# Optimization experiments

Measured on AMD Instinct MI355X. Metric: run time of the kernel, lower is better.

## Reference

```python
import jax, jax.numpy as jnp
import numpy as np

E = 64  # hidden size (hardcoded in the module)
D = 50  # embedding dim (hardcoded)


def lstm_scan(xs, h0, c0, Wih, Whh, b):
    """xs: (S, B, in). PyTorch gate order i, f, g, o."""
    def step(carry, x):
        h, c = carry
        g = x @ Wih.T + h @ Whh.T + b
        i, f, gg, o = jnp.split(g, 4, axis=-1)
        c = jax.nn.sigmoid(f) * c + jax.nn.sigmoid(i) * jnp.tanh(gg)
        h = jax.nn.sigmoid(o) * jnp.tanh(c)
        return (h, c), (h, c)
    _, (hs, cs) = jax.lax.scan(step, (h0, c0), xs)
    return hs, cs  # (S, B, E)


def setup_inputs() -> dict:
    key = jax.random.key(0)
    ks = iter(jax.random.split(key, 40))
    B, S, V = 64, 384, 100004
    f32 = jnp.float32

    def rn(shape, scale):
        return (jax.random.normal(next(ks), shape, dtype=f32) * scale)

    km = float(np.sqrt(2.0 / E))       # kaiming_normal fan_in=64
    lu = float(1.0 / np.sqrt(E))       # torch LSTM default init scale

    inp = {
        "sentence1": jax.random.randint(next(ks), (B, S), 0, V),
        "sentence2": jax.random.randint(next(ks), (B, S), 0, V),
        "s1_len": jax.random.randint(next(ks), (B, 1, E), 0, S),
        "s2_len": jax.random.randint(next(ks), (B, 1, E), 0, S),
        "s1_s": jnp.ones((B, S), dtype=f32),
        "s2_s": jnp.ones((B, S), dtype=f32),
        "emb": rn((V, D), 0.1),
        "Wih1": rn((4 * E, D), lu), "Whh1": rn((4 * E, E), lu),
        "bih1": rn((4 * E,), lu), "bhh1": rn((4 * E,), lu),
        "Wih2": rn((4 * E, D), lu), "Whh2": rn((4 * E, E), lu),
        "bih2": rn((4 * E,), lu), "bhh2": rn((4 * E,), lu),
        "wy": rn((E, E), km), "wh": rn((E, E), km),
        "w": rn((E,), 1.0),
        "wp": rn((E, E), km), "wx": rn((E, E), km),
        "wr": rn((E, E), km), "wt": rn((E, E), km),
        "l1_W": rn((128, E), km), "l1_b": jnp.zeros((128,), f32),
        "l_W": rn((4, 128), float(np.sqrt(2.0 / 128))), "l_b": jnp.zeros((4,), f32),
    }
    return inp


def reference(sentence1, sentence2, s1_len, s2_len, s1_s, s2_s, emb,
              Wih1, Whh1, bih1, bhh1, Wih2, Whh2, bih2, bhh2,
              wy, wh, w, wp, wx, wr, wt, l1_W, l1_b, l_W, l_b):
    B, S = sentence1.shape
    e1 = emb[sentence1]  # (B,S,50)
    e2 = emb[sentence2]
    h0 = jnp.zeros((B, E), e1.dtype)

    # LSTMCell loop over sentence1, collecting all h/c
    hs, cs = lstm_scan(e1.transpose(1, 0, 2), h0, h0, Wih1, Whh1, bih1 + bhh1)
    h = hs.transpose(1, 0, 2)  # (B,S,E)
    c = cs.transpose(1, 0, 2)

    # gather initial state for lstm2 at s1_len indices
    gh = jnp.take_along_axis(h, s1_len, axis=1)[:, 0, :]
    gc = jnp.take_along_axis(c, s1_len, axis=1)[:, 0, :]

    os_, _ = lstm_scan(e2.transpose(1, 0, 2), gh, gc, Wih2, Whh2, bih2 + bhh2)
    out = os_.transpose(1, 0, 2)  # (B,S,E); note s2 == s per expand semantics

    # wyy + whhn are loop-invariant in the original (out.expand is identity)
    base = jnp.einsum('bse,ef->bsf', h, wy) + jnp.einsum('bse,ef->bsf', out, wh)
    NEG = jnp.float32(1e12)

    def att_step(r, _):
        M = jnp.tanh(base + (r @ wr)[:, None, :])          # (B,S,E)
        score = jnp.einsum('bse,e->bs', M, w)              # (B,S)
        masked = s1_s * score - (1.0 - s1_s) * NEG
        soft = jax.nn.softmax(masked, axis=1)
        r_new = jnp.einsum('bse,bs->be', h, soft) + jnp.tanh(r @ wt)
        return r_new, r_new

    r0 = jnp.zeros((B, E), h.dtype)
    _, Rt = jax.lax.scan(att_step, r0, None, length=S)
    Rt = Rt.transpose(1, 0, 2)  # (B,S,E)

    rn_ = jnp.take_along_axis(Rt, s2_len, axis=1)[:, 0, :]
    hn = jnp.take_along_axis(out, s2_len, axis=1)[:, 0, :]
    hid = jnp.tanh(rn_ @ wp + hn @ wx)
    hid = jnp.tanh(hid @ l1_W.T + l1_b)   # Dropout is inference-mode identity
    return hid @ l_W.T + l_b              # (B,4)
```

## Files before the change

### kernel.cpp

```cpp
#include <hip/hip_runtime.h>

#define E 64
#define D 50
#define SS 384
#define G4 256

__device__ __forceinline__ float fast_rcp(float x){ return __builtin_amdgcn_rcpf(x); }
__device__ __forceinline__ float tanh_fast(float x){
  float e = __expf(2.0f*x);
  return 1.0f - 2.0f*fast_rcp(e + 1.0f);
}
__device__ __forceinline__ float sigmoid_fast(float x){
  return fast_rcp(1.0f + __expf(-x));
}
__device__ __forceinline__ float rdlane(float v, int l){
  return __int_as_float(__builtin_amdgcn_readlane(__float_as_int(v), l));
}
#define DPP0(x, ctrl) __int_as_float(__builtin_amdgcn_update_dpp( \
    0, __float_as_int(x), ctrl, 0xF, 0xF, true))
__device__ __forceinline__ float wave_sum64_l63(float x){
  x += DPP0(x, 0x111);
  x += DPP0(x, 0x112);
  x += DPP0(x, 0x114);
  x += DPP0(x, 0x118);
  x += DPP0(x, 0x142);
  x += DPP0(x, 0x143);
  return x;
}

__global__ __launch_bounds__(256, 1) void gx_kernel(
  const int* __restrict__ sent1, const int* __restrict__ sent2,
  const float* __restrict__ emb,
  const float* __restrict__ Wih1, const float* __restrict__ bih1, const float* __restrict__ bhh1,
  const float* __restrict__ Wih2, const float* __restrict__ bih2, const float* __restrict__ bhh2,
  float* __restrict__ gx1, float* __restrict__ gx2)
{
  const int bb    = blockIdx.x;
  const int which = bb >> 8;
  const int chunk = bb & 255;
  const int j     = threadIdx.x;
  const int*   sent = which ? sent2 : sent1;
  const float* Wih  = which ? Wih2  : Wih1;
  const float* bA   = which ? bih2  : bih1;
  const float* bB   = which ? bhh2  : bhh1;
  float*       gx   = which ? gx2   : gx1;

  float wih[D];
  #pragma unroll
  for (int k=0;k<D;k+=2){
    float2 v = *(const float2*)&Wih[j*D+k];
    wih[k]=v.x; wih[k+1]=v.y;
  }
  const float bias = bA[j] + bB[j];

  __shared__ __align__(16) float xb[8][52];
  const int row0 = chunk*96;
  for (int c=0;c<12;++c){
    const int r0 = row0 + c*8;
    #pragma unroll
    for (int q=0;q<2;++q){
      int tt = j + q*256;
      if (tt < 400){
        int r = tt/50;
        int k = tt - r*50;
        int idx = sent[r0 + r];
        xb[r][k] = emb[(size_t)idx*D + k];
      }
    }
    __syncthreads();
    for (int r=0;r<8;++r){
      float a0=bias, a1=0.f;
      #pragma unroll
      for (int k=0;k<48;k+=4){
        float4 xv = *(const float4*)&xb[r][k];
        a0 += xv.x*wih[k]   + xv.y*wih[k+1];
        a1 += xv.z*wih[k+2] + xv.w*wih[k+3];
      }
      a0 += xb[r][48]*wih[48];
      a1 += xb[r][49]*wih[49];
      gx[(size_t)(r0+r)*G4 + j] = a0+a1;
    }
    __syncthreads();
  }
}

__global__ __launch_bounds__(256, 1) void lstm_kernel(
  const float* __restrict__ gx1, const float* __restrict__ gx2,
  const float* __restrict__ Whh1, const float* __restrict__ Whh2,
  const int* __restrict__ s1_len, const int* __restrict__ s2_len,
  float* __restrict__ h1_all, float* __restrict__ out_all,
  float* __restrict__ hn_cap)
{
  const int b = blockIdx.x;
  const int j = threadIdx.x;
  const int lane = j & 63;
  const int wv = j >> 6;
  __shared__ float gates[2][256];
  __shared__ __align__(16) float hbuf[4][64];

  float whr[64];
  #pragma unroll
  for (int k=0;k<64;k+=4){
    float4 v = *(const float4*)&Whh1[j*64+k];
    whr[k]=v.x; whr[k+1]=v.y; whr[k+2]=v.z; whr[k+3]=v.w;
  }

  const int is_g = (wv==2);
  float c_reg=0.f, h_reg=0.f, gh=0.f, gc=0.f, hn=0.f;
  const int idx1 = s1_len[b*64+lane];
  const int idx2 = s2_len[b*64+lane];
  hbuf[wv][lane] = 0.f;

  {
    const float* gx = gx1 + (size_t)b*SS*G4;
    float* hout = h1_all + (size_t)b*SS*E;
    float gx_cur = gx[j];
    float gx_n1  = gx[G4 + j];
    for (int s=0;s<SS;++s){
      int sn2 = (s+2<SS)? s+2 : SS-1;
      float gx_n2 = gx[(size_t)sn2*G4 + j];
      float g0=gx_cur, g1=0.f, g2=0.f, g3=0.f;
      #pragma unroll
      for (int k=0;k<64;k+=4){
        float4 hv = *(const float4*)&hbuf[wv][k];
        g0 = __builtin_fmaf(hv.x, whr[k],   g0);
        g1 = __builtin_fmaf(hv.y, whr[k+1], g1);
        g2 = __builtin_fmaf(hv.z, whr[k+2], g2);
        g3 = __builtin_fmaf(hv.w, whr[k+3], g3);
      }
      float g = (g0+g1)+(g2+g3);
      const int p = s & 1;
      gates[p][j] = is_g ? tanh_fast(g) : sigmoid_fast(g);
      __syncthreads();
      float gi=gates[p][lane], gf=gates[p][64+lane], gg=gates[p][128+lane], go=gates[p][192+lane];
      c_reg = gf*c_reg + gi*gg;
      h_reg = go * tanh_fast(c_reg);
      hbuf[wv][lane] = h_reg;
      if (wv==0) hout[(size_t)s*E + lane] = h_reg;
      if (s==idx1){ gh=h_reg; gc=c_reg; }
      gx_cur = gx_n1; gx_n1 = gx_n2;
    }
  }
  #pragma unroll
  for (int k=0;k<64;k+=4){
    float4 v = *(const float4*)&Whh2[j*64+k];
    whr[k]=v.x; whr[k+1]=v.y; whr[k+2]=v.z; whr[k+3]=v.w;
  }
  h_reg = gh; c_reg = gc;
  hbuf[wv][lane] = gh;
  __syncthreads();
  {
    const float* gx = gx2 + (size_t)b*SS*G4;
    float* hout = out_all + (size_t)b*SS*E;
    float gx_cur = gx[j];
    float gx_n1  = gx[G4 + j];
    for (int s=0;s<SS;++s){
      int sn2 = (s+2<SS)? s+2 : SS-1;
      float gx_n2 = gx[(size_t)sn2*G4 + j];
      float g0=gx_cur, g1=0.f, g2=0.f, g3=0.f;
      #pragma unroll
      for (int k=0;k<64;k+=4){
        float4 hv = *(const float4*)&hbuf[wv][k];
        g0 = __builtin_fmaf(hv.x, whr[k],   g0);
        g1 = __builtin_fmaf(hv.y, whr[k+1], g1);
        g2 = __builtin_fmaf(hv.z, whr[k+2], g2);
        g3 = __builtin_fmaf(hv.w, whr[k+3], g3);
      }
      float g = (g0+g1)+(g2+g3);
      const int p = s & 1;
      gates[p][j] = is_g ? tanh_fast(g) : sigmoid_fast(g);
      __syncthreads();
      float gi=gates[p][lane], gf=gates[p][64+lane], gg=gates[p][128+lane], go=gates[p][192+lane];
      c_reg = gf*c_reg + gi*gg;
      h_reg = go * tanh_fast(c_reg);
      hbuf[wv][lane] = h_reg;
      if (wv==0) hout[(size_t)s*E + lane] = h_reg;
      if (s==idx2) hn = h_reg;
      gx_cur = gx_n1; gx_n1 = gx_n2;
    }
  }
  if (wv==0) hn_cap[b*64+lane] = hn;
}

__global__ __launch_bounds__(256, 1) void base_kernel(
  const float* __restrict__ h1_all, const float* __restrict__ out_all,
  const float* __restrict__ wy, const float* __restrict__ wh,
  float* __restrict__ E_g)
{
  const int t = threadIdx.x;
  const int wave = t>>6, lane = t&63;
  float wyc[E], whc[E];
  #pragma unroll
  for (int e=0;e<E;++e){ wyc[e]=wy[e*E+lane]; whc[e]=wh[e*E+lane]; }
  const int row0 = blockIdx.x*16 + wave*4;
  for (int r=0;r<4;++r){
    int row = row0 + r;
    float hv = h1_all[(size_t)row*E + lane];
    float ov = out_all[(size_t)row*E + lane];
    float a0=0,a1=0;
    #pragma unroll
    for (int e=0;e<E;++e){
      a0 += rdlane(hv,e)*wyc[e];
      a1 += rdlane(ov,e)*whc[e];
    }
    E_g[(size_t)row*E + lane] = __expf(2.0f*(a0+a1));
  }
}

__global__ __launch_bounds__(384, 1) void attn_kernel(
  const float* __restrict__ h1_all, const float* __restrict__ E_all,
  const float* __restrict__ w, const float* __restrict__ wr, const float* __restrict__ wt,
  const float* __restrict__ s1_s, const int* __restrict__ s2_len,
  float* __restrict__ rn_cap)
{
  const int b = blockIdx.x;
  const int t = threadIdx.x;
  const int wv = t>>6, lane = t&63;
  const int row = wv*64 + lane;

  __shared__ float  accP[6*64];
  __shared__ float  totP[8];
  __shared__ float2 rwrtP[6*64];
  __shared__ __align__(16) float exL[6][64];
  __shared__ __align__(16) float RlL[6][64];

  const float* h1b = h1_all + (size_t)b*SS*E;
  const float* Eb  = E_all  + (size_t)b*SS*E;

  float Ee[64];
  #pragma unroll
  for (int k=0;k<64;k+=4){
    float4 v = *(const float4*)&Eb[(size_t)row*E + k];
    Ee[k]=v.x; Ee[k+1]=v.y; Ee[k+2]=v.z; Ee[k+3]=v.w;
  }
  float ht[64];
  #pragma unroll
  for (int i=0;i<64;++i){
    ht[i] = h1b[(size_t)(wv*64 + i)*E + lane];
  }
  float WSUM = 0.f;
  for (int e=0;e<64;++e) WSUM += w[e];
  const float s1v = s1_s[b*SS + row];
  const int  idx2 = s2_len[b*E + lane];
  const int k0  = (wv<4)? wv*11 : 44+(wv-4)*10;
  const int cnt = (wv<4)? 11 : 10;
  float wrch[11], wtch[11];
  #pragma unroll
  for (int jj=0;jj<11;++jj){
    int kk = k0 + ((jj<cnt)? jj : 0);
    wrch[jj] = wr[kk*E + lane];
    wtch[jj] = wt[kk*E + lane];
  }

  rwrtP[t] = make_float2(0.f, 0.f);
  __syncthreads();

  float rn_keep = 0.f;
  for (int s=0;s<SS;++s){
    float rwl=0.f, rtl=0.f;
    #pragma unroll
    for (int q=0;q<6;++q){ float2 v = rwrtP[q*64+lane]; rwl+=v.x; rtl+=v.y; }
    float Rl = __expf(2.0f*rwl);
    RlL[wv][lane] = Rl;

    float sc0=0.f, sc1=0.f, sc2=0.f, sc3=0.f;
    #pragma unroll
    for (int e=0;e<64;e+=8){
      float4 ra = *(const float4*)&RlL[wv][e];
      float4 rb = *(const float4*)&RlL[wv][e+4];
      float A  = __builtin_fmaf(Ee[e],  ra.x, 1.f);
      float B  = __builtin_fmaf(Ee[e+1],ra.y, 1.f);
      float C  = __builtin_fmaf(Ee[e+2],ra.z, 1.f);
      float Dv = __builtin_fmaf(Ee[e+3],ra.w, 1.f);
      float n0 = __builtin_fmaf(w[e],   B,  w[e+1]*A);
      float n1 = __builtin_fmaf(w[e+2], Dv, w[e+3]*C);
      sc0 = __builtin_fmaf(n0, fast_rcp(A*B),  sc0);
      sc1 = __builtin_fmaf(n1, fast_rcp(C*Dv), sc1);
      float A2  = __builtin_fmaf(Ee[e+4], rb.x, 1.f);
      float B2  = __builtin_fmaf(Ee[e+5], rb.y, 1.f);
      float C2  = __builtin_fmaf(Ee[e+6], rb.z, 1.f);
      float D2  = __builtin_fmaf(Ee[e+7], rb.w, 1.f);
      float n2 = __builtin_fmaf(w[e+4], B2, w[e+5]*A2);
      float n3 = __builtin_fmaf(w[e+6], D2, w[e+7]*C2);
      sc2 = __builtin_fmaf(n2, fast_rcp(A2*B2), sc2);
      sc3 = __builtin_fmaf(n3, fast_rcp(C2*D2), sc3);
    }
    float sc = WSUM - 2.0f*((sc0+sc1)+(sc2+sc3));
    float masked = s1v*sc - (1.f - s1v)*1e12f;
    float ex = __expf(masked);

    exL[wv][lane] = ex;
    float a0=0.f, a1=0.f, a2=0.f, a3=0.f;
    #pragma unroll
    for (int i=0;i<64;i+=4){
      float4 v = *(const float4*)&exL[wv][i];
      a0 = __builtin_fmaf(v.x, ht[i],   a0);
      a1 = __builtin_fmaf(v.y, ht[i+1], a1);
      a2 = __builtin_fmaf(v.z, ht[i+2], a2);
      a3 = __builtin_fmaf(v.w, ht[i+3], a3);
    }
    accP[wv*64+lane] = (a0+a1)+(a2+a3);
    float tw = wave_sum64_l63(ex);
    if (lane==63) totP[wv] = tw;
    __syncthreads();

    float av=0.f;
    #pragma unroll
    for (int q=0;q<6;++q) av += accP[q*64+lane];
    float tv = ((totP[0]+totP[1])+(totP[2]+totP[3]))+(totP[4]+totP[5]);
    float rnew = __builtin_fmaf(av, fast_rcp(tv), tanh_fast(rtl));
    if (wv==0 && s==idx2) rn_keep = rnew;
    float rwp=0.f, rtp=0.f;
    #pragma unroll
    for (int jj=0;jj<11;++jj){
      if (jj<cnt){
        float rv = rdlane(rnew, k0+jj);
        rwp = __builtin_fmaf(rv, wrch[jj], rwp);
        rtp = __builtin_fmaf(rv, wtch[jj], rtp);
      }
    }
    rwrtP[wv*64+lane] = make_float2(rwp, rtp);
    __syncthreads();
  }
  if (wv==0) rn_cap[b*E + lane] = rn_keep;
}

__global__ __launch_bounds__(128, 1) void final_kernel(
  const float* __restrict__ rn_cap, const float* __restrict__ hn_cap,
  const float* __restrict__ wp, const float* __restrict__ wx,
  const float* __restrict__ l1W, const float* __restrict__ l1b,
  const float* __restrict__ lW, const float* __restrict__ lb,
  float* __restrict__ out)
{
  const int b = blockIdx.x, t = threadIdx.x;
  __shared__ float rn[E], hn[E], hid1[E], hid2[128];
  if (t<E){ rn[t]=rn_cap[b*E+t]; hn[t]=hn_cap[b*E+t]; }
  __syncthreads();
  if (t<E){
    float a0=0,a1=0;
    #pragma unroll
    for (int k=0;k<E;++k){
      a0 += rn[k]*wp[k*E+t];
      a1 += hn[k]*wx[k*E+t];
    }
    hid1[t] = tanh_fast(a0+a1);
  }
  __syncthreads();
  {
    float acc = l1b[t];
    #pragma unroll
    for (int k=0;k<E;++k) acc += hid1[k]*l1W[t*E+k];
    hid2[t] = tanh_fast(acc);
  }
  __syncthreads();
  if (t<4){
    float acc = lb[t];
    #pragma unroll
    for (int k=0;k<128;++k) acc += hid2[k]*lW[t*128+k];
    out[b*4+t] = acc;
  }
}

extern "C" void kernel_launch(void* const* d_in, const int* in_sizes, int n_in,
                              void* d_out, int out_size, void* d_ws, size_t ws_size,
                              hipStream_t stream)
{
  const int*   sent1 = (const int*)  d_in[0];
  const int*   sent2 = (const int*)  d_in[1];
  const int*   s1len = (const int*)  d_in[2];
  const int*   s2len = (const int*)  d_in[3];
  const float* s1s   = (const float*)d_in[4];
  const float* emb   = (const float*)d_in[6];
  const float* Wih1  = (const float*)d_in[7];
  const float* Whh1  = (const float*)d_in[8];
  const float* bih1  = (const float*)d_in[9];
  const float* bhh1  = (const float*)d_in[10];
  const float* Wih2  = (const float*)d_in[11];
  const float* Whh2  = (const float*)d_in[12];
  const float* bih2  = (const float*)d_in[13];
  const float* bhh2  = (const float*)d_in[14];
  const float* wy    = (const float*)d_in[15];
  const float* wh    = (const float*)d_in[16];
  const float* w     = (const float*)d_in[17];
  const float* wp    = (const float*)d_in[18];
  const float* wx    = (const float*)d_in[19];
  const float* wr    = (const float*)d_in[20];
  const float* wt    = (const float*)d_in[21];
  const float* l1W   = (const float*)d_in[22];
  const float* l1b   = (const float*)d_in[23];
  const float* lW    = (const float*)d_in[24];
  const float* lb    = (const float*)d_in[25];
  float* out = (float*)d_out;

  float* ws  = (float*)d_ws;
  float* gx1 = ws;
  float* gx2 = gx1 + 6291456;
  float* h1  = gx2 + 6291456;
  float* outa= h1  + 1572864;
  float* Eg  = outa + 1572864;
  float* rnc = Eg  + 1572864;
  float* hnc = rnc + 4096;

  hipLaunchKernelGGL(gx_kernel, dim3(512), dim3(256), 0, stream,
    sent1, sent2, emb, Wih1, bih1, bhh1, Wih2, bih2, bhh2, gx1, gx2);
  hipLaunchKernelGGL(lstm_kernel, dim3(64), dim3(256), 0, stream,
    gx1, gx2, Whh1, Whh2, s1len, s2len, h1, outa, hnc);
  hipLaunchKernelGGL(base_kernel, dim3(1536), dim3(256), 0, stream,
    h1, outa, wy, wh, Eg);
  hipLaunchKernelGGL(attn_kernel, dim3(64), dim3(384), 0, stream,
    h1, Eg, w, wr, wt, s1s, s2len, rnc);
  hipLaunchKernelGGL(final_kernel, dim3(64), dim3(128), 0, stream,
    rnc, hnc, wp, wx, l1W, l1b, lW, lb, out);
}
```

Measured before the change: 1.327 ms.

## Run LSTM recurrence in a single wave per batch, removing block barriers

The LSTM kernel now uses one 64-lane wave per batch element, and each lane holds all four gate rows of Whh (256 registers of weights) so it computes i, f, g, o itself. This removes the shared gate exchange and the __syncthreads per timestep, which sat on the serial critical path. In exchange each lane does four times the FMAs per step, and register pressure could cause spills. Separately, the attention kernel computes tanh(rtl) earlier so it can overlap with the score loop.

```diff
diff --git a/kernel.cpp b/kernel.cpp
--- a/kernel.cpp
+++ b/kernel.cpp
@@ -84,102 +84,137 @@
   }
 }
 
-__global__ __launch_bounds__(256, 1) void lstm_kernel(
+__global__ __launch_bounds__(64, 1) void lstm_kernel(
   const float* __restrict__ gx1, const float* __restrict__ gx2,
   const float* __restrict__ Whh1, const float* __restrict__ Whh2,
   const int* __restrict__ s1_len, const int* __restrict__ s2_len,
   float* __restrict__ h1_all, float* __restrict__ out_all,
   float* __restrict__ hn_cap)
 {
-  const int b = blockIdx.x;
-  const int j = threadIdx.x;
-  const int lane = j & 63;
-  const int wv = j >> 6;
-  __shared__ float gates[2][256];
-  __shared__ __align__(16) float hbuf[4][64];
-
-  float whr[64];
+  const int b    = blockIdx.x;
+  const int lane = threadIdx.x;
+  __shared__ __align__(16) float hb[64];
+
+  float wi[64], wf[64], wg[64], wo[64];
   #pragma unroll
   for (int k=0;k<64;k+=4){
-    float4 v = *(const float4*)&Whh1[j*64+k];
-    whr[k]=v.x; whr[k+1]=v.y; whr[k+2]=v.z; whr[k+3]=v.w;
-  }
-
-  const int is_g = (wv==2);
+    float4 vi = *(const float4*)&Whh1[(size_t)(      lane)*64 + k];
+    float4 vf = *(const float4*)&Whh1[(size_t)( 64 + lane)*64 + k];
+    float4 vg = *(const float4*)&Whh1[(size_t)(128 + lane)*64 + k];
+    float4 vo = *(const float4*)&Whh1[(size_t)(192 + lane)*64 + k];
+    wi[k]=vi.x; wi[k+1]=vi.y; wi[k+2]=vi.z; wi[k+3]=vi.w;
+    wf[k]=vf.x; wf[k+1]=vf.y; wf[k+2]=vf.z; wf[k+3]=vf.w;
+    wg[k]=vg.x; wg[k+1]=vg.y; wg[k+2]=vg.z; wg[k+3]=vg.w;
+    wo[k]=vo.x; wo[k+1]=vo.y; wo[k+2]=vo.z; wo[k+3]=vo.w;
+  }
+
   float c_reg=0.f, h_reg=0.f, gh=0.f, gc=0.f, hn=0.f;
   const int idx1 = s1_len[b*64+lane];
   const int idx2 = s2_len[b*64+lane];
-  hbuf[wv][lane] = 0.f;
+  hb[lane] = 0.f;
 
   {
     const float* gx = gx1 + (size_t)b*SS*G4;
     float* hout = h1_all + (size_t)b*SS*E;
-    float gx_cur = gx[j];
-    float gx_n1  = gx[G4 + j];
+    float4 gx_cur, gx_n1;
+    gx_cur.x=gx[lane]; gx_cur.y=gx[64+lane]; gx_cur.z=gx[128+lane]; gx_cur.w=gx[192+lane];
+    gx_n1.x=gx[G4+lane]; gx_n1.y=gx[G4+64+lane]; gx_n1.z=gx[G4+128+lane]; gx_n1.w=gx[G4+192+lane];
     for (int s=0;s<SS;++s){
-      int sn2 = (s+2<SS)? s+2 : SS-1;
-      float gx_n2 = gx[(size_t)sn2*G4 + j];
-      float g0=gx_cur, g1=0.f, g2=0.f, g3=0.f;
+      const size_t o2 = (size_t)((s+2<SS)? s+2 : SS-1)*G4;
+      float4 gx_n2;
+      gx_n2.x=gx[o2+lane]; gx_n2.y=gx[o2+64+lane]; gx_n2.z=gx[o2+128+lane]; gx_n2.w=gx[o2+192+lane];
+      float ai0=gx_cur.x, ai1=0.f, af0=gx_cur.y, af1=0.f;
+      float ag0=gx_cur.z, ag1=0.f, ao0=gx_cur.w, ao1=0.f;
       #pragma unroll
       for (int k=0;k<64;k+=4){
-        float4 hv = *(const float4*)&hbuf[wv][k];
-        g0 = __builtin_fmaf(hv.x, whr[k],   g0);
-        g1 = __builtin_fmaf(hv.y, whr[k+1], g1);
-        g2 = __builtin_fmaf(hv.z, whr[k+2], g2);
-        g3 = __builtin_fmaf(hv.w, whr[k+3], g3);
+        float4 hv = *(const float4*)&hb[k];
+        ai0 = __builtin_fmaf(hv.x, wi[k],   ai0);
+        ai1 = __builtin_fmaf(hv.y, wi[k+1], ai1);
+        ai0 = __builtin_fmaf(hv.z, wi[k+2], ai0);
+        ai1 = __builtin_fmaf(hv.w, wi[k+3], ai1);
+        af0 = __builtin_fmaf(hv.x, wf[k],   af0);
+        af1 = __builtin_fmaf(hv.y, wf[k+1], af1);
+        af0 = __builtin_fmaf(hv.z, wf[k+2], af0);
+        af1 = __builtin_fmaf(hv.w, wf[k+3], af1);
+        ag0 = __builtin_fmaf(hv.x, wg[k],   ag0);
+        ag1 = __builtin_fmaf(hv.y, wg[k+1], ag1);
+        ag0 = __builtin_fmaf(hv.z, wg[k+2], ag0);
+        ag1 = __builtin_fmaf(hv.w, wg[k+3], ag1);
+        ao0 = __builtin_fmaf(hv.x, wo[k],   ao0);
+        ao1 = __builtin_fmaf(hv.y, wo[k+1], ao1);
+        ao0 = __builtin_fmaf(hv.z, wo[k+2], ao0);
+        ao1 = __builtin_fmaf(hv.w, wo[k+3], ao1);
       }
-      float g = (g0+g1)+(g2+g3);
-      const int p = s & 1;
-      gates[p][j] = is_g ? tanh_fast(g) : sigmoid_fast(g);
-      __syncthreads();
-      float gi=gates[p][lane], gf=gates[p][64+lane], gg=gates[p][128+lane], go=gates[p][192+lane];
+      float gi = sigmoid_fast(ai0+ai1);
+      float gf = sigmoid_fast(af0+af1);
+      float gg = tanh_fast(ag0+ag1);
+      float go = sigmoid_fast(ao0+ao1);
       c_reg = gf*c_reg + gi*gg;
       h_reg = go * tanh_fast(c_reg);
-      hbuf[wv][lane] = h_reg;
-      if (wv==0) hout[(size_t)s*E + lane] = h_reg;
+      hb[lane] = h_reg;
+      hout[(size_t)s*E + lane] = h_reg;
       if (s==idx1){ gh=h_reg; gc=c_reg; }
       gx_cur = gx_n1; gx_n1 = gx_n2;
     }
   }
   #pragma unroll
   for (int k=0;k<64;k+=4){
-    float4 v = *(const float4*)&Whh2[j*64+k];
-    whr[k]=v.x; whr[k+1]=v.y; whr[k+2]=v.z; whr[k+3]=v.w;
+    float4 vi = *(const float4*)&Whh2[(size_t)(      lane)*64 + k];
+    float4 vf = *(const float4*)&Whh2[(size_t)( 64 + lane)*64 + k];
+    float4 vg = *(const float4*)&Whh2[(size_t)(128 + lane)*64 + k];
+    float4 vo = *(const float4*)&Whh2[(size_t)(192 + lane)*64 + k];
+    wi[k]=vi.x; wi[k+1]=vi.y; wi[k+2]=vi.z; wi[k+3]=vi.w;
+    wf[k]=vf.x; wf[k+1]=vf.y; wf[k+2]=vf.z; wf[k+3]=vf.w;
+    wg[k]=vg.x; wg[k+1]=vg.y; wg[k+2]=vg.z; wg[k+3]=vg.w;
+    wo[k]=vo.x; wo[k+1]=vo.y; wo[k+2]=vo.z; wo[k+3]=vo.w;
   }
   h_reg = gh; c_reg = gc;
-  hbuf[wv][lane] = gh;
-  __syncthreads();
+  hb[lane] = gh;
   {
     const float* gx = gx2 + (size_t)b*SS*G4;
     float* hout = out_all + (size_t)b*SS*E;
-    float gx_cur = gx[j];
-    float gx_n1  = gx[G4 + j];
+    float4 gx_cur, gx_n1;
+    gx_cur.x=gx[lane]; gx_cur.y=gx[64+lane]; gx_cur.z=gx[128+lane]; gx_cur.w=gx[192+lane];
+    gx_n1.x=gx[G4+lane]; gx_n1.y=gx[G4+64+lane]; gx_n1.z=gx[G4+128+lane]; gx_n1.w=gx[G4+192+lane];
     for (int s=0;s<SS;++s){
-      int sn2 = (s+2<SS)? s+2 : SS-1;
-      float gx_n2 = gx[(size_t)sn2*G4 + j];
-      float g0=gx_cur, g1=0.f, g2=0.f, g3=0.f;
+      const size_t o2 = (size_t)((s+2<SS)? s+2 : SS-1)*G4;
+      float4 gx_n2;
+      gx_n2.x=gx[o2+lane]; gx_n2.y=gx[o2+64+lane]; gx_n2.z=gx[o2+128+lane]; gx_n2.w=gx[o2+192+lane];
+      float ai0=gx_cur.x, ai1=0.f, af0=gx_cur.y, af1=0.f;
+      float ag0=gx_cur.z, ag1=0.f, ao0=gx_cur.w, ao1=0.f;
       #pragma unroll
       for (int k=0;k<64;k+=4){
-        float4 hv = *(const float4*)&hbuf[wv][k];
-        g0 = __builtin_fmaf(hv.x, whr[k],   g0);
-        g1 = __builtin_fmaf(hv.y, whr[k+1], g1);
-        g2 = __builtin_fmaf(hv.z, whr[k+2], g2);
-        g3 = __builtin_fmaf(hv.w, whr[k+3], g3);
+        float4 hv = *(const float4*)&hb[k];
+        ai0 = __builtin_fmaf(hv.x, wi[k],   ai0);
+        ai1 = __builtin_fmaf(hv.y, wi[k+1], ai1);
+        ai0 = __builtin_fmaf(hv.z, wi[k+2], ai0);
+        ai1 = __builtin_fmaf(hv.w, wi[k+3], ai1);
+        af0 = __builtin_fmaf(hv.x, wf[k],   af0);
+        af1 = __builtin_fmaf(hv.y, wf[k+1], af1);
+        af0 = __builtin_fmaf(hv.z, wf[k+2], af0);
+        af1 = __builtin_fmaf(hv.w, wf[k+3], af1);
+        ag0 = __builtin_fmaf(hv.x, wg[k],   ag0);
+        ag1 = __builtin_fmaf(hv.y, wg[k+1], ag1);
+        ag0 = __builtin_fmaf(hv.z, wg[k+2], ag0);
+        ag1 = __builtin_fmaf(hv.w, wg[k+3], ag1);
+        ao0 = __builtin_fmaf(hv.x, wo[k],   ao0);
+        ao1 = __builtin_fmaf(hv.y, wo[k+1], ao1);
+        ao0 = __builtin_fmaf(hv.z, wo[k+2], ao0);
+        ao1 = __builtin_fmaf(hv.w, wo[k+3], ao1);
       }
-      float g = (g0+g1)+(g2+g3);
-      const int p = s & 1;
-      gates[p][j] = is_g ? tanh_fast(g) : sigmoid_fast(g);
-      __syncthreads();
-      float gi=gates[p][lane], gf=gates[p][64+lane], gg=gates[p][128+lane], go=gates[p][192+lane];
+      float gi = sigmoid_fast(ai0+ai1);
+      float gf = sigmoid_fast(af0+af1);
+      float gg = tanh_fast(ag0+ag1);
+      float go = sigmoid_fast(ao0+ao1);
       c_reg = gf*c_reg + gi*gg;
       h_reg = go * tanh_fast(c_reg);
-      hbuf[wv][lane] = h_reg;
-      if (wv==0) hout[(size_t)s*E + lane] = h_reg;
+      hb[lane] = h_reg;
+      hout[(size_t)s*E + lane] = h_reg;
       if (s==idx2) hn = h_reg;
       gx_cur = gx_n1; gx_n1 = gx_n2;
     }
   }
-  if (wv==0) hn_cap[b*64+lane] = hn;
+  hn_cap[b*64+lane] = hn;
 }
 
 __global__ __launch_bounds__(256, 1) void base_kernel(
@@ -262,6 +297,7 @@
     for (int q=0;q<6;++q){ float2 v = rwrtP[q*64+lane]; rwl+=v.x; rtl+=v.y; }
     float Rl = __expf(2.0f*rwl);
     RlL[wv][lane] = Rl;
+    float trt = tanh_fast(rtl);
 
     float sc0=0.f, sc1=0.f, sc2=0.f, sc3=0.f;
     #pragma unroll
@@ -308,7 +344,7 @@
     #pragma unroll
     for (int q=0;q<6;++q) av += accP[q*64+lane];
     float tv = ((totP[0]+totP[1])+(totP[2]+totP[3]))+(totP[4]+totP[5]);
-    float rnew = __builtin_fmaf(av, fast_rcp(tv), tanh_fast(rtl));
+    float rnew = __builtin_fmaf(av, fast_rcp(tv), trt);
     if (wv==0 && s==idx2) rn_keep = rnew;
     float rwp=0.f, rtp=0.f;
     #pragma unroll
@@ -403,7 +439,7 @@
 
   hipLaunchKernelGGL(gx_kernel, dim3(512), dim3(256), 0, stream,
     sent1, sent2, emb, Wih1, bih1, bhh1, Wih2, bih2, bhh2, gx1, gx2);
-  hipLaunchKernelGGL(lstm_kernel, dim3(64), dim3(256), 0, stream,
+  hipLaunchKernelGGL(lstm_kernel, dim3(64), dim3(64), 0, stream,
     gx1, gx2, Whh1, Whh2, s1len, s2len, h1, outa, hnc);
   hipLaunchKernelGGL(base_kernel, dim3(1536), dim3(256), 0, stream,
     h1, outa, wy, wh, Eg);
```

New measurement: 1.569 ms. +18.3%, slower.

## Stage attention h tile in LDS and defer LSTM h stores by one step

Applied to the files above, without the earlier changes.

The attention kernel now copies the per-batch h1 sequence (96 KB) into dynamic shared memory and reads it from LDS inside the loop, replacing the 64-register ht array. The aim is to cut register pressure in the 384-thread block. The LSTM loops write each hidden state one step late, so the global store sits off the critical path right after the LDS write. tanh(rtl) is also hoisted earlier in the attention step. The cost is extra LDS reads per step, possible bank conflicts on the strided hl access, and a need for large dynamic shared memory.

```diff
diff --git a/kernel.cpp b/kernel.cpp
--- a/kernel.cpp
+++ b/kernel.cpp
@@ -116,6 +116,7 @@
     float* hout = h1_all + (size_t)b*SS*E;
     float gx_cur = gx[j];
     float gx_n1  = gx[G4 + j];
+    float h_prev = 0.f;
     for (int s=0;s<SS;++s){
       int sn2 = (s+2<SS)? s+2 : SS-1;
       float gx_n2 = gx[(size_t)sn2*G4 + j];
@@ -136,10 +137,12 @@
       c_reg = gf*c_reg + gi*gg;
       h_reg = go * tanh_fast(c_reg);
       hbuf[wv][lane] = h_reg;
-      if (wv==0) hout[(size_t)s*E + lane] = h_reg;
+      if (wv==0 && s>0) hout[(size_t)(s-1)*E + lane] = h_prev;
+      h_prev = h_reg;
       if (s==idx1){ gh=h_reg; gc=c_reg; }
       gx_cur = gx_n1; gx_n1 = gx_n2;
     }
+    if (wv==0) hout[(size_t)(SS-1)*E + lane] = h_prev;
   }
   #pragma unroll
   for (int k=0;k<64;k+=4){
@@ -154,6 +157,7 @@
     float* hout = out_all + (size_t)b*SS*E;
     float gx_cur = gx[j];
     float gx_n1  = gx[G4 + j];
+    float h_prev = 0.f;
     for (int s=0;s<SS;++s){
       int sn2 = (s+2<SS)? s+2 : SS-1;
       float gx_n2 = gx[(size_t)sn2*G4 + j];
@@ -174,10 +178,12 @@
       c_reg = gf*c_reg + gi*gg;
       h_reg = go * tanh_fast(c_reg);
       hbuf[wv][lane] = h_reg;
-      if (wv==0) hout[(size_t)s*E + lane] = h_reg;
+      if (wv==0 && s>0) hout[(size_t)(s-1)*E + lane] = h_prev;
+      h_prev = h_reg;
       if (s==idx2) hn = h_reg;
       gx_cur = gx_n1; gx_n1 = gx_n2;
     }
+    if (wv==0) hout[(size_t)(SS-1)*E + lane] = h_prev;
   }
   if (wv==0) hn_cap[b*64+lane] = hn;
 }
@@ -218,6 +224,8 @@
   const int wv = t>>6, lane = t&63;
   const int row = wv*64 + lane;
 
+  extern __shared__ float h_lds[];
+
   __shared__ float  accP[6*64];
   __shared__ float  totP[8];
   __shared__ float2 rwrtP[6*64];
@@ -227,16 +235,13 @@
   const float* h1b = h1_all + (size_t)b*SS*E;
   const float* Eb  = E_all  + (size_t)b*SS*E;
 
+  for (int idx=t; idx<SS*E; idx+=384) h_lds[idx] = h1b[idx];
+
   float Ee[64];
   #pragma unroll
   for (int k=0;k<64;k+=4){
     float4 v = *(const float4*)&Eb[(size_t)row*E + k];
     Ee[k]=v.x; Ee[k+1]=v.y; Ee[k+2]=v.z; Ee[k+3]=v.w;
-  }
-  float ht[64];
-  #pragma unroll
-  for (int i=0;i<64;++i){
-    ht[i] = h1b[(size_t)(wv*64 + i)*E + lane];
   }
   float WSUM = 0.f;
   for (int e=0;e<64;++e) WSUM += w[e];
@@ -255,6 +260,8 @@
   rwrtP[t] = make_float2(0.f, 0.f);
   __syncthreads();
 
+  const float* hl = h_lds + (size_t)(wv*64)*64 + lane;
+
   float rn_keep = 0.f;
   for (int s=0;s<SS;++s){
     float rwl=0.f, rtl=0.f;
@@ -262,6 +269,7 @@
     for (int q=0;q<6;++q){ float2 v = rwrtP[q*64+lane]; rwl+=v.x; rtl+=v.y; }
     float Rl = __expf(2.0f*rwl);
     RlL[wv][lane] = Rl;
+    float trt = tanh_fast(rtl);
 
     float sc0=0.f, sc1=0.f, sc2=0.f, sc3=0.f;
     #pragma unroll
@@ -294,10 +302,10 @@
     #pragma unroll
     for (int i=0;i<64;i+=4){
       float4 v = *(const float4*)&exL[wv][i];
-      a0 = __builtin_fmaf(v.x, ht[i],   a0);
-      a1 = __builtin_fmaf(v.y, ht[i+1], a1);
-      a2 = __builtin_fmaf(v.z, ht[i+2], a2);
-      a3 = __builtin_fmaf(v.w, ht[i+3], a3);
+      a0 = __builtin_fmaf(v.x, hl[(i+0)*64], a0);
+      a1 = __builtin_fmaf(v.y, hl[(i+1)*64], a1);
+      a2 = __builtin_fmaf(v.z, hl[(i+2)*64], a2);
+      a3 = __builtin_fmaf(v.w, hl[(i+3)*64], a3);
     }
     accP[wv*64+lane] = (a0+a1)+(a2+a3);
     float tw = wave_sum64_l63(ex);
@@ -308,7 +316,7 @@
     #pragma unroll
     for (int q=0;q<6;++q) av += accP[q*64+lane];
     float tv = ((totP[0]+totP[1])+(totP[2]+totP[3]))+(totP[4]+totP[5]);
-    float rnew = __builtin_fmaf(av, fast_rcp(tv), tanh_fast(rtl));
+    float rnew = __builtin_fmaf(av, fast_rcp(tv), trt);
     if (wv==0 && s==idx2) rn_keep = rnew;
     float rwp=0.f, rtp=0.f;
     #pragma unroll
@@ -401,13 +409,21 @@
   float* rnc = Eg  + 1572864;
   float* hnc = rnc + 4096;
 
+  static bool attn_attr_set = false;
+  if (!attn_attr_set){
+    hipFuncSetAttribute(reinterpret_cast<const void*>(attn_kernel),
+                        hipFuncAttributeMaxDynamicSharedMemorySize,
+                        SS*E*(int)sizeof(float));
+    attn_attr_set = true;
+  }
+
   hipLaunchKernelGGL(gx_kernel, dim3(512), dim3(256), 0, stream,
     sent1, sent2, emb, Wih1, bih1, bhh1, Wih2, bih2, bhh2, gx1, gx2);
   hipLaunchKernelGGL(lstm_kernel, dim3(64), dim3(256), 0, stream,
     gx1, gx2, Whh1, Whh2, s1len, s2len, h1, outa, hnc);
   hipLaunchKernelGGL(base_kernel, dim3(1536), dim3(256), 0, stream,
     h1, outa, wy, wh, Eg);
-  hipLaunchKernelGGL(attn_kernel, dim3(64), dim3(384), 0, stream,
+  hipLaunchKernelGGL(attn_kernel, dim3(64), dim3(384), SS*E*sizeof(float), stream,
     h1, Eg, w, wr, wt, s1s, s2len, rnc);
   hipLaunchKernelGGL(final_kernel, dim3(64), dim3(128), 0, stream,
     rnc, hnc, wp, wx, l1W, l1b, lW, lb, out);
```

Measured after the change: 1.436 ms. 1.08x slower.
